# Performance work log

Hardware: AMD Instinct MI355X
Metric: run time of the kernel (lower is better)

## Reference

```python
import jax, jax.numpy as jnp
import numpy as np

B, L, H, E = 2, 2048, 8, 64
S = L  # self-attention


def setup_inputs() -> dict:
    key = jax.random.key(0)
    k1, k2, k3, k4, k5 = jax.random.split(key, 5)
    return {
        "queries": jax.random.normal(k1, (B, L, H, E), dtype=jnp.float32),
        "keys": jax.random.normal(k2, (B, S, H, E), dtype=jnp.float32),
        "values": jax.random.normal(k3, (B, S, H, E), dtype=jnp.float32),
        "tau": jax.random.uniform(k4, (B, 1), dtype=jnp.float32),
        "delta": jax.random.normal(k5, (B, S), dtype=jnp.float32),
    }


def reference(queries, keys, values, tau, delta):
    # De-stationary attention: scores = (QK^T) * tau + delta, causal mask, softmax, AV
    E_ = queries.shape[-1]
    scale = 1.0 / jnp.sqrt(jnp.float32(E_))
    tau_b = tau[:, None, None, :]      # [B,1,1,1]
    delta_b = delta[:, None, None, :]  # [B,1,1,S]
    scores = jnp.einsum('blhe,bshe->bhls', queries, keys) * tau_b + delta_b  # [B,H,L,S]
    Lq, Sk = scores.shape[-2], scores.shape[-1]
    causal = jnp.triu(jnp.ones((Lq, Sk), dtype=bool), k=1)  # True = masked
    scores = jnp.where(causal[None, None], -jnp.inf, scores)
    A = jax.nn.softmax(scale * scores, axis=-1)
    V = jnp.einsum('bhls,bshd->blhd', A, values)
    return V
```

## Files before the change

kernel.cpp:

```cpp
#include <hip/hip_runtime.h>


typedef _Float16 h8 __attribute__((ext_vector_type(8)));
typedef _Float16 h2 __attribute__((ext_vector_type(2)));
typedef float f32x4 __attribute__((ext_vector_type(4)));

constexpr int Bc = 2, Lc = 2048, Hc = 8, Ec = 64, Sc = 2048;
constexpr int QT = 64, KT = 64;
constexpr int LDK = 72;
constexpr float SCALE = 0.125f;
constexpr float LOG2E = 1.44269504088896340736f;

__device__ __forceinline__ h2 pk2(float x, float y) {
  return __builtin_bit_cast(h2, __builtin_amdgcn_cvt_pkrtz(x, y));
}

template <int CTRL>
__device__ __forceinline__ float dpp_f(float x) {
  int r = __builtin_amdgcn_update_dpp(0, __builtin_bit_cast(int, x), CTRL, 0xF, 0xF, true);
  return __builtin_bit_cast(float, r);
}
__device__ __forceinline__ float rowmax16(float x) {
  x = fmaxf(x, dpp_f<0xB1>(x));
  x = fmaxf(x, dpp_f<0x4E>(x));
  x = fmaxf(x, dpp_f<0x124>(x));
  x = fmaxf(x, dpp_f<0x128>(x));
  return x;
}

__global__ __launch_bounds__(256, 2)
void dsattn(const float* __restrict__ Qg, const float* __restrict__ Kg,
            const float* __restrict__ Vg, const float* __restrict__ taug,
            const float* __restrict__ deltag, float* __restrict__ Og) {
  __shared__ __align__(16) _Float16 Ks[2][KT * LDK];
  __shared__ __align__(16) _Float16 Vt[2][Ec * LDK];
  __shared__ __align__(16) _Float16 Pb[4][16 * LDK];

  const int tid = threadIdx.x;
  const int wave = tid >> 6, lane = tid & 63;
  const int quad = lane >> 4, l16 = lane & 15;

  const int q_tile = (int)gridDim.x - 1 - (int)blockIdx.x;
  const int q0 = q_tile * QT;
  const int b = (int)blockIdx.y >> 3, h = (int)blockIdx.y & 7;

  const float ct = taug[b] * (SCALE * LOG2E);

  const int qm = q0 + (wave << 4) + l16;
  const float* qp = Qg + (((size_t)b * Lc + qm) * Hc + h) * Ec;
  h8 qfrag[2];
#pragma unroll
  for (int kk = 0; kk < 2; ++kk) {
    float4 a0 = ((const float4*)(qp + quad * 8 + kk * 32))[0];
    float4 a1 = ((const float4*)(qp + quad * 8 + kk * 32))[1];
    union { h8 v; h2 p[4]; } u;
    u.p[0] = pk2(a0.x, a0.y); u.p[1] = pk2(a0.z, a0.w);
    u.p[2] = pk2(a1.x, a1.y); u.p[3] = pk2(a1.z, a1.w);
    qfrag[kk] = u.v;
  }

  h8 onesf;
#pragma unroll
  for (int j = 0; j < 8; ++j) onesf[j] = (_Float16)1.0f;

  f32x4 Oacc[4], Osum;
#pragma unroll
  for (int nt = 0; nt < 4; ++nt) Oacc[nt] = (f32x4){0.f, 0.f, 0.f, 0.f};
  Osum = (f32x4){0.f, 0.f, 0.f, 0.f};
  float mrow[4];
#pragma unroll
  for (int r = 0; r < 4; ++r) mrow[r] = -1e30f;

  const int srow = tid >> 2;
  const int sec = (tid & 3) << 4;
  const int vrp = ((tid >> 3) + 4 * (tid & 7)) & 31;
  const int ve8 = (tid & 7) << 3;

  _Float16* pb = &Pb[wave][0];

  float dcur[4];

  {
    const float* kp = Kg + (((size_t)b * Sc + srow) * Hc + h) * Ec + sec;
    float4 c0 = ((const float4*)kp)[0], c1 = ((const float4*)kp)[1];
    float4 c2 = ((const float4*)kp)[2], c3 = ((const float4*)kp)[3];
    const float* vp0 = Vg + (((size_t)b * Sc + 2 * vrp) * Hc + h) * Ec + ve8;
    const float* vp1 = vp0 + Hc * Ec;
    float4 r00 = ((const float4*)vp0)[0], r01 = ((const float4*)vp0)[1];
    float4 r10 = ((const float4*)vp1)[0], r11 = ((const float4*)vp1)[1];
#pragma unroll
    for (int nt = 0; nt < 4; ++nt)
      dcur[nt] = deltag[(size_t)b * Sc + nt * 16 + l16] * (SCALE * LOG2E);
    union { h8 v; h2 p[4]; } w0, w1;
    w0.p[0] = pk2(c0.x, c0.y); w0.p[1] = pk2(c0.z, c0.w);
    w0.p[2] = pk2(c1.x, c1.y); w0.p[3] = pk2(c1.z, c1.w);
    w1.p[0] = pk2(c2.x, c2.y); w1.p[1] = pk2(c2.z, c2.w);
    w1.p[2] = pk2(c3.x, c3.y); w1.p[3] = pk2(c3.z, c3.w);
    *(h8*)&Ks[0][srow * LDK + sec] = w0.v;
    *(h8*)&Ks[0][srow * LDK + sec + 8] = w1.v;
    const float e0[8] = {r00.x, r00.y, r00.z, r00.w, r01.x, r01.y, r01.z, r01.w};
    const float e1[8] = {r10.x, r10.y, r10.z, r10.w, r11.x, r11.y, r11.z, r11.w};
#pragma unroll
    for (int j = 0; j < 8; ++j)
      *(h2*)&Vt[0][(ve8 + j) * LDK + 2 * vrp] = pk2(e0[j], e1[j]);
  }

  for (int kt = 0; kt <= q_tile; ++kt) {
    const int cur = kt & 1;
    const bool pf = (kt < q_tile);

    float4 kn0, kn1, kn2, kn3, vn00, vn01, vn10, vn11;
    float dn[4];
    if (pf) {
      const int nb = (kt + 1) * KT;
      const float* kp = Kg + (((size_t)b * Sc + nb + srow) * Hc + h) * Ec + sec;
      kn0 = ((const float4*)kp)[0]; kn1 = ((const float4*)kp)[1];
      kn2 = ((const float4*)kp)[2]; kn3 = ((const float4*)kp)[3];
      const float* vp0 = Vg + (((size_t)b * Sc + nb + 2 * vrp) * Hc + h) * Ec + ve8;
      const float* vp1 = vp0 + Hc * Ec;
      vn00 = ((const float4*)vp0)[0]; vn01 = ((const float4*)vp0)[1];
      vn10 = ((const float4*)vp1)[0]; vn11 = ((const float4*)vp1)[1];
#pragma unroll
      for (int nt = 0; nt < 4; ++nt)
        dn[nt] = deltag[(size_t)b * Sc + nb + nt * 16 + l16];
    }

    __syncthreads();

    f32x4 Sacc[4];
#pragma unroll
    for (int nt = 0; nt < 4; ++nt) Sacc[nt] = (f32x4){0.f, 0.f, 0.f, 0.f};
#pragma unroll
    for (int kk = 0; kk < 2; ++kk) {
#pragma unroll
      for (int nt = 0; nt < 4; ++nt) {
        h8 bf = *(const h8*)&Ks[cur][(nt * 16 + l16) * LDK + quad * 8 + kk * 32];
        Sacc[nt] = __builtin_amdgcn_mfma_f32_16x16x32_f16(qfrag[kk], bf, Sacc[nt], 0, 0, 0);
      }
    }

    const int kbase = kt * KT;
    const int qr0 = q0 + (wave << 4) + (quad << 2);
    const bool diag = (kt == q_tile);
    float sv[4][4];
#pragma unroll
    for (int nt = 0; nt < 4; ++nt) {
      const int key = kbase + nt * 16 + l16;
#pragma unroll
      for (int r = 0; r < 4; ++r) {
        float s = Sacc[nt][r] * ct + dcur[nt];
        sv[nt][r] = (!diag || key <= qr0 + r) ? s : -1e30f;
      }
    }

    float alpha[4];
#pragma unroll
    for (int r = 0; r < 4; ++r) {
      float t = fmaxf(fmaxf(sv[0][r], sv[1][r]), fmaxf(sv[2][r], sv[3][r]));
      t = rowmax16(t);
      float mn = fmaxf(mrow[r], t);
      alpha[r] = __builtin_amdgcn_exp2f(mrow[r] - mn);
      mrow[r] = mn;
    }
#pragma unroll
    for (int nt = 0; nt < 4; ++nt)
#pragma unroll
      for (int r = 0; r < 4; ++r)
        sv[nt][r] = __builtin_amdgcn_exp2f(sv[nt][r] - mrow[r]);

#pragma unroll
    for (int nt = 0; nt < 4; ++nt)
#pragma unroll
      for (int r = 0; r < 4; ++r) Oacc[nt][r] *= alpha[r];
#pragma unroll
    for (int r = 0; r < 4; ++r) Osum[r] *= alpha[r];

    {
      const int lo = l16 & 1;
      const int base = (lo ? 32 : 0) + (l16 & ~1);
#pragma unroll
      for (int r = 0; r < 4; ++r) {
        float o0 = dpp_f<0xB1>(sv[0][r]);
        float o1 = dpp_f<0xB1>(sv[1][r]);
        float o2 = dpp_f<0xB1>(sv[2][r]);
        float o3 = dpp_f<0xB1>(sv[3][r]);
        h2 d0 = pk2(lo ? o2 : sv[0][r], lo ? sv[2][r] : o0);
        h2 d1 = pk2(lo ? o3 : sv[1][r], lo ? sv[3][r] : o1);
        _Float16* pp = &pb[((quad << 2) + r) * LDK + base];
        *(h2*)pp = d0;
        *(h2*)(pp + 16) = d1;
      }
    }
    asm volatile("s_waitcnt lgkmcnt(0)" ::: "memory");

#pragma unroll
    for (int kk = 0; kk < 2; ++kk) {
      h8 af = *(const h8*)&pb[l16 * LDK + quad * 8 + kk * 32];
#pragma unroll
      for (int nt = 0; nt < 4; ++nt) {
        h8 vf = *(const h8*)&Vt[cur][(nt * 16 + l16) * LDK + quad * 8 + kk * 32];
        Oacc[nt] = __builtin_amdgcn_mfma_f32_16x16x32_f16(af, vf, Oacc[nt], 0, 0, 0);
      }
      Osum = __builtin_amdgcn_mfma_f32_16x16x32_f16(af, onesf, Osum, 0, 0, 0);
    }

    if (pf) {
      _Float16* ksn = &Ks[cur ^ 1][0];
      _Float16* vtn = &Vt[cur ^ 1][0];
      union { h8 v; h2 p[4]; } w0, w1;
      w0.p[0] = pk2(kn0.x, kn0.y); w0.p[1] = pk2(kn0.z, kn0.w);
      w0.p[2] = pk2(kn1.x, kn1.y); w0.p[3] = pk2(kn1.z, kn1.w);
      w1.p[0] = pk2(kn2.x, kn2.y); w1.p[1] = pk2(kn2.z, kn2.w);
      w1.p[2] = pk2(kn3.x, kn3.y); w1.p[3] = pk2(kn3.z, kn3.w);
      *(h8*)&ksn[srow * LDK + sec] = w0.v;
      *(h8*)&ksn[srow * LDK + sec + 8] = w1.v;
      const float e0[8] = {vn00.x, vn00.y, vn00.z, vn00.w, vn01.x, vn01.y, vn01.z, vn01.w};
      const float e1[8] = {vn10.x, vn10.y, vn10.z, vn10.w, vn11.x, vn11.y, vn11.z, vn11.w};
#pragma unroll
      for (int j = 0; j < 8; ++j)
        *(h2*)&vtn[(ve8 + j) * LDK + 2 * vrp] = pk2(e0[j], e1[j]);
#pragma unroll
      for (int nt = 0; nt < 4; ++nt) dcur[nt] = dn[nt] * (SCALE * LOG2E);
    }
  }

#pragma unroll
  for (int r = 0; r < 4; ++r) {
    const int qrow = q0 + (wave << 4) + (quad << 2) + r;
    const float inv = 1.0f / Osum[r];
    float* op = Og + (((size_t)b * Lc + qrow) * Hc + h) * Ec;
#pragma unroll
    for (int nt = 0; nt < 4; ++nt) op[nt * 16 + l16] = Oacc[nt][r] * inv;
  }
}

extern "C" void kernel_launch(void* const* d_in, const int* in_sizes, int n_in,
                              void* d_out, int out_size, void* d_ws, size_t ws_size,
                              hipStream_t stream) {
  const float* Q = (const float*)d_in[0];
  const float* K = (const float*)d_in[1];
  const float* V = (const float*)d_in[2];
  const float* tau = (const float*)d_in[3];
  const float* delta = (const float*)d_in[4];
  float* O = (float*)d_out;
  dim3 grid(Lc / QT, Bc * Hc);
  dsattn<<<grid, 256, 0, stream>>>(Q, K, V, tau, delta, O);
}
```

Before: 126.7 us.

## Split causal KV range into chunks with partial outputs and a combine kernel

Each query tile's key range is split into chunks of up to 8 key tiles, each handled by its own block. Partial O, max and sum are written to workspace, and a second kernel merges them with log-sum-exp rescaling. This balances the triangular causal workload across many more blocks and raises occupancy to 3 blocks per SM. The cost is an extra launch, round-trips of partial data through global memory, and many early-exit blocks. If the workspace is too small, it falls back to the original single-pass path.

```diff
diff --git a/kernel.cpp b/kernel.cpp
--- a/kernel.cpp
+++ b/kernel.cpp
@@ -7,6 +7,7 @@
 
 constexpr int Bc = 2, Lc = 2048, Hc = 8, Ec = 64, Sc = 2048;
 constexpr int QT = 64, KT = 64;
+constexpr int NQT = Lc / QT;
 constexpr int LDK = 72;
 constexpr float SCALE = 0.125f;
 constexpr float LOG2E = 1.44269504088896340736f;
@@ -28,21 +29,31 @@
   return x;
 }
 
-__global__ __launch_bounds__(256, 2)
-void dsattn(const float* __restrict__ Qg, const float* __restrict__ Kg,
-            const float* __restrict__ Vg, const float* __restrict__ taug,
-            const float* __restrict__ deltag, float* __restrict__ Og) {
+template <int CH, int EPB>
+__global__ __launch_bounds__(256, 3)
+void dsattn_fwd(const float* __restrict__ Qg, const float* __restrict__ Kg,
+                const float* __restrict__ Vg, const float* __restrict__ taug,
+                const float* __restrict__ deltag, float* __restrict__ Og,
+                float* __restrict__ Opart, float* __restrict__ Mpart,
+                float* __restrict__ Lpart) {
   __shared__ __align__(16) _Float16 Ks[2][KT * LDK];
   __shared__ __align__(16) _Float16 Vt[2][Ec * LDK];
   __shared__ __align__(16) _Float16 Pb[4][16 * LDK];
 
+  const int bx = (int)blockIdx.x;
+  int qt, c0;
+  if (CH >= NQT) { qt = NQT - 1 - bx; c0 = 0; }
+  else { qt = NQT - 1 - (bx >> 2); c0 = bx & 3; if (c0 * CH > qt) return; }
+  const int nch = qt / CH + 1;
+  const int ktBeg = c0 * CH;
+  const int ktEnd = (qt < ktBeg + CH - 1) ? qt : (ktBeg + CH - 1);
+
   const int tid = threadIdx.x;
   const int wave = tid >> 6, lane = tid & 63;
   const int quad = lane >> 4, l16 = lane & 15;
-
-  const int q_tile = (int)gridDim.x - 1 - (int)blockIdx.x;
-  const int q0 = q_tile * QT;
-  const int b = (int)blockIdx.y >> 3, h = (int)blockIdx.y & 7;
+  const int q0 = qt * QT;
+  const int bh = (int)blockIdx.y;
+  const int b = bh >> 3, h = bh & 7;
 
   const float ct = taug[b] * (SCALE * LOG2E);
 
@@ -77,25 +88,25 @@
   const int ve8 = (tid & 7) << 3;
 
   _Float16* pb = &Pb[wave][0];
-
   float dcur[4];
 
   {
-    const float* kp = Kg + (((size_t)b * Sc + srow) * Hc + h) * Ec + sec;
-    float4 c0 = ((const float4*)kp)[0], c1 = ((const float4*)kp)[1];
-    float4 c2 = ((const float4*)kp)[2], c3 = ((const float4*)kp)[3];
-    const float* vp0 = Vg + (((size_t)b * Sc + 2 * vrp) * Hc + h) * Ec + ve8;
+    const int kb = ktBeg * KT;
+    const float* kp = Kg + (((size_t)b * Sc + kb + srow) * Hc + h) * Ec + sec;
+    float4 c0v = ((const float4*)kp)[0], c1v = ((const float4*)kp)[1];
+    float4 c2v = ((const float4*)kp)[2], c3v = ((const float4*)kp)[3];
+    const float* vp0 = Vg + (((size_t)b * Sc + kb + 2 * vrp) * Hc + h) * Ec + ve8;
     const float* vp1 = vp0 + Hc * Ec;
     float4 r00 = ((const float4*)vp0)[0], r01 = ((const float4*)vp0)[1];
     float4 r10 = ((const float4*)vp1)[0], r11 = ((const float4*)vp1)[1];
 #pragma unroll
     for (int nt = 0; nt < 4; ++nt)
-      dcur[nt] = deltag[(size_t)b * Sc + nt * 16 + l16] * (SCALE * LOG2E);
+      dcur[nt] = deltag[(size_t)b * Sc + kb + nt * 16 + l16] * (SCALE * LOG2E);
     union { h8 v; h2 p[4]; } w0, w1;
-    w0.p[0] = pk2(c0.x, c0.y); w0.p[1] = pk2(c0.z, c0.w);
-    w0.p[2] = pk2(c1.x, c1.y); w0.p[3] = pk2(c1.z, c1.w);
-    w1.p[0] = pk2(c2.x, c2.y); w1.p[1] = pk2(c2.z, c2.w);
-    w1.p[2] = pk2(c3.x, c3.y); w1.p[3] = pk2(c3.z, c3.w);
+    w0.p[0] = pk2(c0v.x, c0v.y); w0.p[1] = pk2(c0v.z, c0v.w);
+    w0.p[2] = pk2(c1v.x, c1v.y); w0.p[3] = pk2(c1v.z, c1v.w);
+    w1.p[0] = pk2(c2v.x, c2v.y); w1.p[1] = pk2(c2v.z, c2v.w);
+    w1.p[2] = pk2(c3v.x, c3v.y); w1.p[3] = pk2(c3v.z, c3v.w);
     *(h8*)&Ks[0][srow * LDK + sec] = w0.v;
     *(h8*)&Ks[0][srow * LDK + sec + 8] = w1.v;
     const float e0[8] = {r00.x, r00.y, r00.z, r00.w, r01.x, r01.y, r01.z, r01.w};
@@ -105,9 +116,9 @@
       *(h2*)&Vt[0][(ve8 + j) * LDK + 2 * vrp] = pk2(e0[j], e1[j]);
   }
 
-  for (int kt = 0; kt <= q_tile; ++kt) {
-    const int cur = kt & 1;
-    const bool pf = (kt < q_tile);
+  for (int kt = ktBeg; kt <= ktEnd; ++kt) {
+    const int cur = (kt - ktBeg) & 1;
+    const bool pf = (kt < ktEnd);
 
     float4 kn0, kn1, kn2, kn3, vn00, vn01, vn10, vn11;
     float dn[4];
@@ -141,7 +152,7 @@
 
     const int kbase = kt * KT;
     const int qr0 = q0 + (wave << 4) + (quad << 2);
-    const bool diag = (kt == q_tile);
+    const bool diag = (kt == qt);
     float sv[4][4];
 #pragma unroll
     for (int nt = 0; nt < 4; ++nt) {
@@ -224,13 +235,79 @@
     }
   }
 
-#pragma unroll
-  for (int r = 0; r < 4; ++r) {
-    const int qrow = q0 + (wave << 4) + (quad << 2) + r;
-    const float inv = 1.0f / Osum[r];
-    float* op = Og + (((size_t)b * Lc + qrow) * Hc + h) * Ec;
-#pragma unroll
-    for (int nt = 0; nt < 4; ++nt) op[nt * 16 + l16] = Oacc[nt][r] * inv;
+  if (nch == 1) {
+#pragma unroll
+    for (int r = 0; r < 4; ++r) {
+      const int qrow = q0 + (wave << 4) + (quad << 2) + r;
+      const float inv = 1.0f / Osum[r];
+      float* op = Og + (((size_t)b * Lc + qrow) * Hc + h) * Ec;
+#pragma unroll
+      for (int nt = 0; nt < 4; ++nt) op[nt * 16 + l16] = Oacc[nt][r] * inv;
+    }
+  } else {
+    const int g = qt / CH, rem = qt - g * CH;
+    const int pre = qt + CH * (g * (g - 1) / 2) + rem * g;
+    const int e = bh * EPB + pre + c0;
+    float* op = Opart + (size_t)e * (QT * Ec);
+#pragma unroll
+    for (int r = 0; r < 4; ++r) {
+      const int row = (wave << 4) + (quad << 2) + r;
+#pragma unroll
+      for (int nt = 0; nt < 4; ++nt)
+        op[row * Ec + nt * 16 + l16] = Oacc[nt][r];
+      if (l16 == 0) {
+        Mpart[e * QT + row] = mrow[r];
+        Lpart[e * QT + row] = Osum[r];
+      }
+    }
+  }
+}
+
+template <int CH, int EPB>
+__global__ __launch_bounds__(256, 4)
+void dsattn_comb(const float* __restrict__ Opart, const float* __restrict__ Mpart,
+                 const float* __restrict__ Lpart, float* __restrict__ Og) {
+  const int qt = CH + (int)blockIdx.x;
+  const int bh = (int)blockIdx.y;
+  const int b = bh >> 3, h = bh & 7;
+  const int nch = qt / CH + 1;
+  const int row = threadIdx.x >> 2;
+  const int colg = (threadIdx.x & 3) << 4;
+
+  const int g = qt / CH, rem = qt - g * CH;
+  const int pre = qt + CH * (g * (g - 1) / 2) + rem * g;
+  const int e0 = bh * EPB + pre;
+
+  float ms[4];
+  float M = -1e30f;
+  for (int c = 0; c < nch; ++c) {
+    ms[c] = Mpart[(e0 + c) * QT + row];
+    M = fmaxf(M, ms[c]);
+  }
+  float acc[16];
+#pragma unroll
+  for (int i = 0; i < 16; ++i) acc[i] = 0.f;
+  float l = 0.f;
+  for (int c = 0; c < nch; ++c) {
+    const float w = __builtin_amdgcn_exp2f(ms[c] - M);
+    l += w * Lpart[(e0 + c) * QT + row];
+    const float* op = Opart + (size_t)(e0 + c) * (QT * Ec) + row * Ec + colg;
+#pragma unroll
+    for (int i = 0; i < 4; ++i) {
+      float4 v = ((const float4*)op)[i];
+      acc[4 * i + 0] += w * v.x; acc[4 * i + 1] += w * v.y;
+      acc[4 * i + 2] += w * v.z; acc[4 * i + 3] += w * v.w;
+    }
+  }
+  const float inv = 1.0f / l;
+  const int qrow = qt * QT + row;
+  float* out = Og + (((size_t)b * Lc + qrow) * Hc + h) * Ec + colg;
+#pragma unroll
+  for (int i = 0; i < 4; ++i) {
+    float4 v;
+    v.x = acc[4 * i + 0] * inv; v.y = acc[4 * i + 1] * inv;
+    v.z = acc[4 * i + 2] * inv; v.w = acc[4 * i + 3] * inv;
+    ((float4*)out)[i] = v;
   }
 }
 
@@ -243,6 +320,24 @@
   const float* tau = (const float*)d_in[3];
   const float* delta = (const float*)d_in[4];
   float* O = (float*)d_out;
-  dim3 grid(Lc / QT, Bc * Hc);
-  dsattn<<<grid, 256, 0, stream>>>(Q, K, V, tau, delta, O);
-}
+
+  constexpr int CH = 8;
+  constexpr int EPB = 80;
+  constexpr int TOT_E = Bc * Hc * EPB;
+  const size_t need = (size_t)TOT_E * QT * Ec * 4 + 2 * (size_t)TOT_E * QT * 4;
+
+  if (ws_size >= need) {
+    float* Opart = (float*)d_ws;
+    float* Mpart = Opart + (size_t)TOT_E * QT * Ec;
+    float* Lpart = Mpart + (size_t)TOT_E * QT;
+    dim3 g1(NQT * 4, Bc * Hc);
+    dsattn_fwd<CH, EPB><<<g1, 256, 0, stream>>>(Q, K, V, tau, delta, O,
+                                                Opart, Mpart, Lpart);
+    dim3 g2(NQT - CH, Bc * Hc);
+    dsattn_comb<CH, EPB><<<g2, 256, 0, stream>>>(Opart, Mpart, Lpart, O);
+  } else {
+    dim3 g1(NQT, Bc * Hc);
+    dsattn_fwd<NQT, NQT><<<g1, 256, 0, stream>>>(Q, K, V, tau, delta, O,
+                                                 nullptr, nullptr, nullptr);
+  }
+}
```

Measured after the change: 129.6 us. 1.02x slower.

## Split causal attention along keys into chunks with per-wave query rows and a combine pass

Applied to the files above, without the earlier changes.

Each wave now handles its own 16-row query strip and reads K and V fragments straight from global memory into registers. The LDS double-buffering and block-wide barriers are gone. The key range is split into chunks of 512 keys spread across extra blocks (split-K, flash-decoding style). Partial outputs, maxes and sums go to workspace and a second kernel merges them, which evens out the causal triangle load and raises parallelism. The cost is more global traffic, since K and V are re-read per wave instead of shared through LDS, plus a second launch and a workspace round trip.

```diff
diff --git a/kernel.cpp b/kernel.cpp
--- a/kernel.cpp
+++ b/kernel.cpp
@@ -6,15 +6,15 @@
 typedef float f32x4 __attribute__((ext_vector_type(4)));
 
 constexpr int Bc = 2, Lc = 2048, Hc = 8, Ec = 64, Sc = 2048;
-constexpr int QT = 64, KT = 64;
-constexpr int LDK = 72;
+constexpr int QS = 16;
+constexpr int NSUB = Lc / QS;
+constexpr int LDP = 40;
 constexpr float SCALE = 0.125f;
 constexpr float LOG2E = 1.44269504088896340736f;
 
 __device__ __forceinline__ h2 pk2(float x, float y) {
   return __builtin_bit_cast(h2, __builtin_amdgcn_cvt_pkrtz(x, y));
 }
-
 template <int CTRL>
 __device__ __forceinline__ float dpp_f(float x) {
   int r = __builtin_amdgcn_update_dpp(0, __builtin_bit_cast(int, x), CTRL, 0xF, 0xF, true);
@@ -27,36 +27,46 @@
   x = fmaxf(x, dpp_f<0x128>(x));
   return x;
 }
-
-__global__ __launch_bounds__(256, 2)
-void dsattn(const float* __restrict__ Qg, const float* __restrict__ Kg,
-            const float* __restrict__ Vg, const float* __restrict__ taug,
-            const float* __restrict__ deltag, float* __restrict__ Og) {
-  __shared__ __align__(16) _Float16 Ks[2][KT * LDK];
-  __shared__ __align__(16) _Float16 Vt[2][Ec * LDK];
-  __shared__ __align__(16) _Float16 Pb[4][16 * LDK];
-
+__device__ __forceinline__ h8 pack8(float4 a, float4 b) {
+  union { h8 v; h2 p[4]; } u;
+  u.p[0] = pk2(a.x, a.y); u.p[1] = pk2(a.z, a.w);
+  u.p[2] = pk2(b.x, b.y); u.p[3] = pk2(b.z, b.w);
+  return u.v;
+}
+
+template <int CSTEPS, int EPB>
+__global__ __launch_bounds__(256, 4)
+void dsattn_fwd(const float* __restrict__ Qg, const float* __restrict__ Kg,
+                const float* __restrict__ Vg, const float* __restrict__ taug,
+                const float* __restrict__ deltag, float* __restrict__ Og,
+                float* __restrict__ Opart, float* __restrict__ Mpart,
+                float* __restrict__ Lpart) {
+  __shared__ __align__(16) _Float16 Pb[4][16 * LDP];
+
+  constexpr bool SP = (CSTEPS < 128);
   const int tid = threadIdx.x;
   const int wave = tid >> 6, lane = tid & 63;
   const int quad = lane >> 4, l16 = lane & 15;
 
-  const int q_tile = (int)gridDim.x - 1 - (int)blockIdx.x;
-  const int q0 = q_tile * QT;
-  const int b = (int)blockIdx.y >> 3, h = (int)blockIdx.y & 7;
-
+  const int gx = (int)blockIdx.x;
+  const int qgrp = SP ? (gx >> 2) : gx;
+  const int c0 = SP ? (gx & 3) : 0;
+  const int qsub = NSUB - 1 - (qgrp * 4 + wave);
+  const int nch = (qsub * QS + 15) / (CSTEPS * 32) + 1;
+  if (c0 >= nch) return;
+
+  const int q0 = qsub * QS;
+  const int bh = (int)blockIdx.y;
+  const int b = bh >> 3, h = bh & 7;
   const float ct = taug[b] * (SCALE * LOG2E);
-
-  const int qm = q0 + (wave << 4) + l16;
-  const float* qp = Qg + (((size_t)b * Lc + qm) * Hc + h) * Ec;
+  const float cd = SCALE * LOG2E;
+
+  const float* qp = Qg + (((size_t)b * Lc + q0 + l16) * Hc + h) * Ec + quad * 8;
   h8 qfrag[2];
 #pragma unroll
   for (int kk = 0; kk < 2; ++kk) {
-    float4 a0 = ((const float4*)(qp + quad * 8 + kk * 32))[0];
-    float4 a1 = ((const float4*)(qp + quad * 8 + kk * 32))[1];
-    union { h8 v; h2 p[4]; } u;
-    u.p[0] = pk2(a0.x, a0.y); u.p[1] = pk2(a0.z, a0.w);
-    u.p[2] = pk2(a1.x, a1.y); u.p[3] = pk2(a1.z, a1.w);
-    qfrag[kk] = u.v;
+    const float4* p = (const float4*)(qp + kk * 32);
+    qfrag[kk] = pack8(p[0], p[1]);
   }
 
   h8 onesf;
@@ -71,167 +81,155 @@
 #pragma unroll
   for (int r = 0; r < 4; ++r) mrow[r] = -1e30f;
 
-  const int srow = tid >> 2;
-  const int sec = (tid & 3) << 4;
-  const int vrp = ((tid >> 3) + 4 * (tid & 7)) & 31;
-  const int ve8 = (tid & 7) << 3;
+  const int kbeg = c0 * CSTEPS * 32;
+  const int kend = min(kbeg + CSTEPS * 32 - 1, q0 + QS - 1);
+  const int nst = (kend - kbeg) / 32 + 1;
+
+  const float* kp = Kg + (((size_t)b * Sc + kbeg + l16) * Hc + h) * Ec + quad * 8;
+  const float* vp = Vg + (((size_t)b * Sc + kbeg + quad * 8) * Hc + h) * Ec + l16;
+  const float* dp = deltag + (size_t)b * Sc + kbeg + l16;
 
   _Float16* pb = &Pb[wave][0];
-
-  float dcur[4];
-
-  {
-    const float* kp = Kg + (((size_t)b * Sc + srow) * Hc + h) * Ec + sec;
-    float4 c0 = ((const float4*)kp)[0], c1 = ((const float4*)kp)[1];
-    float4 c2 = ((const float4*)kp)[2], c3 = ((const float4*)kp)[3];
-    const float* vp0 = Vg + (((size_t)b * Sc + 2 * vrp) * Hc + h) * Ec + ve8;
-    const float* vp1 = vp0 + Hc * Ec;
-    float4 r00 = ((const float4*)vp0)[0], r01 = ((const float4*)vp0)[1];
-    float4 r10 = ((const float4*)vp1)[0], r11 = ((const float4*)vp1)[1];
-#pragma unroll
-    for (int nt = 0; nt < 4; ++nt)
-      dcur[nt] = deltag[(size_t)b * Sc + nt * 16 + l16] * (SCALE * LOG2E);
-    union { h8 v; h2 p[4]; } w0, w1;
-    w0.p[0] = pk2(c0.x, c0.y); w0.p[1] = pk2(c0.z, c0.w);
-    w0.p[2] = pk2(c1.x, c1.y); w0.p[3] = pk2(c1.z, c1.w);
-    w1.p[0] = pk2(c2.x, c2.y); w1.p[1] = pk2(c2.z, c2.w);
-    w1.p[2] = pk2(c3.x, c3.y); w1.p[3] = pk2(c3.z, c3.w);
-    *(h8*)&Ks[0][srow * LDK + sec] = w0.v;
-    *(h8*)&Ks[0][srow * LDK + sec + 8] = w1.v;
-    const float e0[8] = {r00.x, r00.y, r00.z, r00.w, r01.x, r01.y, r01.z, r01.w};
-    const float e1[8] = {r10.x, r10.y, r10.z, r10.w, r11.x, r11.y, r11.z, r11.w};
+  const int lo = l16 & 1;
+  const int colb = (l16 & ~1) + (lo ? 16 : 0);
+
+  for (int t = 0; t < nst; ++t) {
+    const int kb = kbeg + t * 32;
+
+    h8 kf[2][2];
+#pragma unroll
+    for (int g = 0; g < 2; ++g)
+#pragma unroll
+      for (int kk = 0; kk < 2; ++kk) {
+        const float4* p = (const float4*)(kp + g * (16 * 512) + kk * 32);
+        kf[g][kk] = pack8(p[0], p[1]);
+      }
+
+    float vv[4][8];
 #pragma unroll
     for (int j = 0; j < 8; ++j)
-      *(h2*)&Vt[0][(ve8 + j) * LDK + 2 * vrp] = pk2(e0[j], e1[j]);
-  }
-
-  for (int kt = 0; kt <= q_tile; ++kt) {
-    const int cur = kt & 1;
-    const bool pf = (kt < q_tile);
-
-    float4 kn0, kn1, kn2, kn3, vn00, vn01, vn10, vn11;
-    float dn[4];
-    if (pf) {
-      const int nb = (kt + 1) * KT;
-      const float* kp = Kg + (((size_t)b * Sc + nb + srow) * Hc + h) * Ec + sec;
-      kn0 = ((const float4*)kp)[0]; kn1 = ((const float4*)kp)[1];
-      kn2 = ((const float4*)kp)[2]; kn3 = ((const float4*)kp)[3];
-      const float* vp0 = Vg + (((size_t)b * Sc + nb + 2 * vrp) * Hc + h) * Ec + ve8;
-      const float* vp1 = vp0 + Hc * Ec;
-      vn00 = ((const float4*)vp0)[0]; vn01 = ((const float4*)vp0)[1];
-      vn10 = ((const float4*)vp1)[0]; vn11 = ((const float4*)vp1)[1];
-#pragma unroll
-      for (int nt = 0; nt < 4; ++nt)
-        dn[nt] = deltag[(size_t)b * Sc + nb + nt * 16 + l16];
-    }
-
-    __syncthreads();
-
-    f32x4 Sacc[4];
-#pragma unroll
-    for (int nt = 0; nt < 4; ++nt) Sacc[nt] = (f32x4){0.f, 0.f, 0.f, 0.f};
+#pragma unroll
+      for (int nt = 0; nt < 4; ++nt) vv[nt][j] = vp[j * 512 + nt * 16];
+
+    const float dt0 = dp[0] * cd, dt1 = dp[16] * cd;
+
+    f32x4 Sacc[2] = {(f32x4){0.f, 0.f, 0.f, 0.f}, (f32x4){0.f, 0.f, 0.f, 0.f}};
 #pragma unroll
     for (int kk = 0; kk < 2; ++kk) {
-#pragma unroll
-      for (int nt = 0; nt < 4; ++nt) {
-        h8 bf = *(const h8*)&Ks[cur][(nt * 16 + l16) * LDK + quad * 8 + kk * 32];
-        Sacc[nt] = __builtin_amdgcn_mfma_f32_16x16x32_f16(qfrag[kk], bf, Sacc[nt], 0, 0, 0);
+      Sacc[0] = __builtin_amdgcn_mfma_f32_16x16x32_f16(qfrag[kk], kf[0][kk], Sacc[0], 0, 0, 0);
+      Sacc[1] = __builtin_amdgcn_mfma_f32_16x16x32_f16(qfrag[kk], kf[1][kk], Sacc[1], 0, 0, 0);
+    }
+
+    float sv[2][4];
+#pragma unroll
+    for (int g = 0; g < 2; ++g)
+#pragma unroll
+      for (int r = 0; r < 4; ++r)
+        sv[g][r] = Sacc[g][r] * ct + (g ? dt1 : dt0);
+
+    if (kb + 31 > q0) {
+#pragma unroll
+      for (int g = 0; g < 2; ++g) {
+        const int key = kb + g * 16 + l16;
+#pragma unroll
+        for (int r = 0; r < 4; ++r)
+          if (key > q0 + quad * 4 + r) sv[g][r] = -1e30f;
       }
     }
 
-    const int kbase = kt * KT;
-    const int qr0 = q0 + (wave << 4) + (quad << 2);
-    const bool diag = (kt == q_tile);
-    float sv[4][4];
+#pragma unroll
+    for (int r = 0; r < 4; ++r) {
+      float tm = rowmax16(fmaxf(sv[0][r], sv[1][r]));
+      float mn = fmaxf(mrow[r], tm);
+      float alpha = __builtin_amdgcn_exp2f(mrow[r] - mn);
+      mrow[r] = mn;
+      sv[0][r] = __builtin_amdgcn_exp2f(sv[0][r] - mn);
+      sv[1][r] = __builtin_amdgcn_exp2f(sv[1][r] - mn);
+      Osum[r] *= alpha;
+#pragma unroll
+      for (int nt = 0; nt < 4; ++nt) Oacc[nt][r] *= alpha;
+    }
+
+#pragma unroll
+    for (int r = 0; r < 4; ++r) {
+      float o0 = dpp_f<0xB1>(sv[0][r]);
+      float o1 = dpp_f<0xB1>(sv[1][r]);
+      h2 d = lo ? pk2(o1, sv[1][r]) : pk2(sv[0][r], o0);
+      *(h2*)&pb[(quad * 4 + r) * LDP + colb] = d;
+    }
+    asm volatile("s_waitcnt lgkmcnt(0)" ::: "memory");
+    h8 af = *(const h8*)&pb[l16 * LDP + quad * 8];
+
 #pragma unroll
     for (int nt = 0; nt < 4; ++nt) {
-      const int key = kbase + nt * 16 + l16;
-#pragma unroll
-      for (int r = 0; r < 4; ++r) {
-        float s = Sacc[nt][r] * ct + dcur[nt];
-        sv[nt][r] = (!diag || key <= qr0 + r) ? s : -1e30f;
+      h8 vf = pack8((float4){vv[nt][0], vv[nt][1], vv[nt][2], vv[nt][3]},
+                    (float4){vv[nt][4], vv[nt][5], vv[nt][6], vv[nt][7]});
+      Oacc[nt] = __builtin_amdgcn_mfma_f32_16x16x32_f16(af, vf, Oacc[nt], 0, 0, 0);
+    }
+    Osum = __builtin_amdgcn_mfma_f32_16x16x32_f16(af, onesf, Osum, 0, 0, 0);
+
+    kp += 32 * 512; vp += 32 * 512; dp += 32;
+  }
+
+  if (nch == 1) {
+#pragma unroll
+    for (int r = 0; r < 4; ++r) {
+      const float inv = 1.0f / Osum[r];
+      float* op = Og + (((size_t)b * Lc + q0 + quad * 4 + r) * Hc + h) * Ec;
+#pragma unroll
+      for (int nt = 0; nt < 4; ++nt) op[nt * 16 + l16] = Oacc[nt][r] * inv;
+    }
+  } else {
+    const int g = qsub >> 5, rem = qsub & 31;
+    const int pre = qsub + 32 * (g * (g - 1) / 2) + rem * g;
+    const int e = bh * EPB + pre + c0;
+    float* op = Opart + (size_t)e * (QS * Ec);
+#pragma unroll
+    for (int r = 0; r < 4; ++r) {
+      const int row = quad * 4 + r;
+#pragma unroll
+      for (int nt = 0; nt < 4; ++nt) op[row * Ec + nt * 16 + l16] = Oacc[nt][r];
+      if (l16 == 0) {
+        Mpart[e * QS + row] = mrow[r];
+        Lpart[e * QS + row] = Osum[r];
       }
     }
-
-    float alpha[4];
-#pragma unroll
-    for (int r = 0; r < 4; ++r) {
-      float t = fmaxf(fmaxf(sv[0][r], sv[1][r]), fmaxf(sv[2][r], sv[3][r]));
-      t = rowmax16(t);
-      float mn = fmaxf(mrow[r], t);
-      alpha[r] = __builtin_amdgcn_exp2f(mrow[r] - mn);
-      mrow[r] = mn;
-    }
-#pragma unroll
-    for (int nt = 0; nt < 4; ++nt)
-#pragma unroll
-      for (int r = 0; r < 4; ++r)
-        sv[nt][r] = __builtin_amdgcn_exp2f(sv[nt][r] - mrow[r]);
-
-#pragma unroll
-    for (int nt = 0; nt < 4; ++nt)
-#pragma unroll
-      for (int r = 0; r < 4; ++r) Oacc[nt][r] *= alpha[r];
-#pragma unroll
-    for (int r = 0; r < 4; ++r) Osum[r] *= alpha[r];
-
-    {
-      const int lo = l16 & 1;
-      const int base = (lo ? 32 : 0) + (l16 & ~1);
-#pragma unroll
-      for (int r = 0; r < 4; ++r) {
-        float o0 = dpp_f<0xB1>(sv[0][r]);
-        float o1 = dpp_f<0xB1>(sv[1][r]);
-        float o2 = dpp_f<0xB1>(sv[2][r]);
-        float o3 = dpp_f<0xB1>(sv[3][r]);
-        h2 d0 = pk2(lo ? o2 : sv[0][r], lo ? sv[2][r] : o0);
-        h2 d1 = pk2(lo ? o3 : sv[1][r], lo ? sv[3][r] : o1);
-        _Float16* pp = &pb[((quad << 2) + r) * LDK + base];
-        *(h2*)pp = d0;
-        *(h2*)(pp + 16) = d1;
-      }
-    }
-    asm volatile("s_waitcnt lgkmcnt(0)" ::: "memory");
-
-#pragma unroll
-    for (int kk = 0; kk < 2; ++kk) {
-      h8 af = *(const h8*)&pb[l16 * LDK + quad * 8 + kk * 32];
-#pragma unroll
-      for (int nt = 0; nt < 4; ++nt) {
-        h8 vf = *(const h8*)&Vt[cur][(nt * 16 + l16) * LDK + quad * 8 + kk * 32];
-        Oacc[nt] = __builtin_amdgcn_mfma_f32_16x16x32_f16(af, vf, Oacc[nt], 0, 0, 0);
-      }
-      Osum = __builtin_amdgcn_mfma_f32_16x16x32_f16(af, onesf, Osum, 0, 0, 0);
-    }
-
-    if (pf) {
-      _Float16* ksn = &Ks[cur ^ 1][0];
-      _Float16* vtn = &Vt[cur ^ 1][0];
-      union { h8 v; h2 p[4]; } w0, w1;
-      w0.p[0] = pk2(kn0.x, kn0.y); w0.p[1] = pk2(kn0.z, kn0.w);
-      w0.p[2] = pk2(kn1.x, kn1.y); w0.p[3] = pk2(kn1.z, kn1.w);
-      w1.p[0] = pk2(kn2.x, kn2.y); w1.p[1] = pk2(kn2.z, kn2.w);
-      w1.p[2] = pk2(kn3.x, kn3.y); w1.p[3] = pk2(kn3.z, kn3.w);
-      *(h8*)&ksn[srow * LDK + sec] = w0.v;
-      *(h8*)&ksn[srow * LDK + sec + 8] = w1.v;
-      const float e0[8] = {vn00.x, vn00.y, vn00.z, vn00.w, vn01.x, vn01.y, vn01.z, vn01.w};
-      const float e1[8] = {vn10.x, vn10.y, vn10.z, vn10.w, vn11.x, vn11.y, vn11.z, vn11.w};
-#pragma unroll
-      for (int j = 0; j < 8; ++j)
-        *(h2*)&vtn[(ve8 + j) * LDK + 2 * vrp] = pk2(e0[j], e1[j]);
-#pragma unroll
-      for (int nt = 0; nt < 4; ++nt) dcur[nt] = dn[nt] * (SCALE * LOG2E);
-    }
-  }
-
-#pragma unroll
-  for (int r = 0; r < 4; ++r) {
-    const int qrow = q0 + (wave << 4) + (quad << 2) + r;
-    const float inv = 1.0f / Osum[r];
-    float* op = Og + (((size_t)b * Lc + qrow) * Hc + h) * Ec;
-#pragma unroll
-    for (int nt = 0; nt < 4; ++nt) op[nt * 16 + l16] = Oacc[nt][r] * inv;
-  }
+  }
+}
+
+template <int EPB>
+__global__ __launch_bounds__(256, 8)
+void dsattn_comb(const float* __restrict__ Opart, const float* __restrict__ Mpart,
+                 const float* __restrict__ Lpart, float* __restrict__ Og) {
+  const int qsub = 32 + (int)blockIdx.x;
+  const int bh = (int)blockIdx.y;
+  const int b = bh >> 3, h = bh & 7;
+  const int nch = (qsub >> 5) + 1;
+  const int row = threadIdx.x >> 4;
+  const int c4 = (threadIdx.x & 15) << 2;
+
+  const int g = qsub >> 5, rem = qsub & 31;
+  const int pre = qsub + 32 * (g * (g - 1) / 2) + rem * g;
+  const int e0 = bh * EPB + pre;
+
+  float ms[4];
+  float M = -1e30f;
+  for (int c = 0; c < nch; ++c) {
+    ms[c] = Mpart[(e0 + c) * QS + row];
+    M = fmaxf(M, ms[c]);
+  }
+  float4 acc = {0.f, 0.f, 0.f, 0.f};
+  float l = 0.f;
+  for (int c = 0; c < nch; ++c) {
+    const float w = __builtin_amdgcn_exp2f(ms[c] - M);
+    l += w * Lpart[(e0 + c) * QS + row];
+    float4 v = *(const float4*)(Opart + (size_t)(e0 + c) * (QS * Ec) + row * Ec + c4);
+    acc.x += w * v.x; acc.y += w * v.y; acc.z += w * v.z; acc.w += w * v.w;
+  }
+  const float inv = 1.0f / l;
+  float* out = Og + (((size_t)b * Lc + qsub * QS + row) * Hc + h) * Ec + c4;
+  float4 o; o.x = acc.x * inv; o.y = acc.y * inv; o.z = acc.z * inv; o.w = acc.w * inv;
+  *(float4*)out = o;
 }
 
 extern "C" void kernel_launch(void* const* d_in, const int* in_sizes, int n_in,
@@ -243,6 +241,23 @@
   const float* tau = (const float*)d_in[3];
   const float* delta = (const float*)d_in[4];
   float* O = (float*)d_out;
-  dim3 grid(Lc / QT, Bc * Hc);
-  dsattn<<<grid, 256, 0, stream>>>(Q, K, V, tau, delta, O);
-}
+
+  constexpr int EPB = 320;
+  constexpr int TOT_E = Bc * Hc * EPB;
+  const size_t need = (size_t)TOT_E * QS * Ec * 4 + 2 * (size_t)TOT_E * QS * 4;
+
+  if (ws_size >= need) {
+    float* Opart = (float*)d_ws;
+    float* Mpart = Opart + (size_t)TOT_E * QS * Ec;
+    float* Lpart = Mpart + (size_t)TOT_E * QS;
+    dim3 g1(32 * 4, Bc * Hc);
+    dsattn_fwd<16, EPB><<<g1, 256, 0, stream>>>(Q, K, V, tau, delta, O,
+                                                Opart, Mpart, Lpart);
+    dim3 g2(NSUB - 32, Bc * Hc);
+    dsattn_comb<EPB><<<g2, 256, 0, stream>>>(Opart, Mpart, Lpart, O);
+  } else {
+    dim3 g1(32, Bc * Hc);
+    dsattn_fwd<128, 1><<<g1, 256, 0, stream>>>(Q, K, V, tau, delta, O,
+                                               nullptr, nullptr, nullptr);
+  }
+}
```

New measurement: 228.1 us. 80.0% more time.
